# Kernel optimization log

Measured on AMD Instinct MI355X. Metric: run time of the kernel, lower is better.

The kernel has to match this reference:

```python
import jax, jax.numpy as jnp
import numpy as np

HID = 512
HEADS = 8
HEAD_DIM = HID // HEADS
B, S = 2, 4096


def setup_inputs() -> dict:
    key = jax.random.key(0)
    ks = jax.random.split(key, 11)
    sc = 0.02
    return {
        "query": jax.random.normal(ks[0], (B, S, HID), jnp.float32),
        "key": jax.random.normal(ks[1], (B, S, HID), jnp.float32),
        "value": jax.random.normal(ks[2], (B, S, HID), jnp.float32),
        "Wq": jax.random.normal(ks[3], (HID, HID), jnp.float32) * sc,
        "bq": jax.random.normal(ks[4], (HID,), jnp.float32) * sc,
        "Wk": jax.random.normal(ks[5], (HID, HID), jnp.float32) * sc,
        "bk": jax.random.normal(ks[6], (HID,), jnp.float32) * sc,
        "Wv": jax.random.normal(ks[7], (HID, HID), jnp.float32) * sc,
        "bv": jax.random.normal(ks[8], (HID,), jnp.float32) * sc,
        "Wo": jax.random.normal(ks[9], (HID, HID), jnp.float32) * sc,
        "bo": jax.random.normal(ks[10], (HID,), jnp.float32) * sc,
    }


def reference(query, key, value, Wq, bq, Wk, bk, Wv, bv, Wo, bo):
    b, s, _ = query.shape
    scale = jnp.sqrt(jnp.float32(HEAD_DIM))
    # projections (nn.Linear: x @ W.T + b)
    Q = query @ Wq.T + bq
    K = key @ Wk.T + bk
    V = value @ Wv.T + bv
    # split heads: [b, h, s, d]
    Q = Q.reshape(b, s, HEADS, HEAD_DIM).transpose(0, 2, 1, 3)
    K = K.reshape(b, s, HEADS, HEAD_DIM).transpose(0, 2, 1, 3)
    V = V.reshape(b, s, HEADS, HEAD_DIM).transpose(0, 2, 1, 3)
    # scaled dot-product attention (mask=None, dropout in eval mode = identity)
    energy = jnp.einsum('bhqd,bhkd->bhqk', Q, K) / scale
    attention = jax.nn.softmax(energy, axis=-1)
    x = jnp.einsum('bhqk,bhkd->bhqd', attention, V)
    x = x.transpose(0, 2, 1, 3).reshape(b, s, HID)
    return x @ Wo.T + bo
```

## Files before the change

### kernel.cpp

```cpp
#include <hip/hip_runtime.h>
#include <stdint.h>

#define HID 512
#define NH 8
#define HD 64
#define BATCH 2
#define SEQ 4096
#define M_TOT (BATCH*SEQ)
#define NBH (BATCH*NH)
#define SPLITK 4

typedef __attribute__((ext_vector_type(8))) short short8;
typedef __attribute__((ext_vector_type(4))) short short4v;
typedef __attribute__((ext_vector_type(4))) float floatx4;
typedef unsigned short u16;

__device__ inline u16 f2bf(float x) {
  unsigned u = __builtin_bit_cast(unsigned, x);
  unsigned r = u + 0x7fff + ((u >> 16) & 1);
  return (u16)(r >> 16);
}

__device__ inline float bf2f(u16 h) {
  unsigned u = ((unsigned)h) << 16;
  return __builtin_bit_cast(float, u);
}

__device__ inline unsigned pack_bf16(float a, float b) {
  unsigned ua = __builtin_bit_cast(unsigned, a) + 0x8000u;
  unsigned ub = __builtin_bit_cast(unsigned, b) + 0x8000u;
  return __builtin_amdgcn_perm(ub, ua, 0x07060302u);
}

__device__ inline void gll16(const void* g, void* l) {
  __builtin_amdgcn_global_load_lds((const __attribute__((address_space(1))) void*)g,
                                   (__attribute__((address_space(3))) void*)l, 16, 0, 0);
}


__global__ void cvt_all(const float* __restrict__ q, const float* __restrict__ k,
                        const float* __restrict__ v, const float* __restrict__ wq,
                        const float* __restrict__ wk, const float* __restrict__ wv,
                        const float* __restrict__ wo,
                        u16* __restrict__ xq, u16* __restrict__ xk,
                        u16* __restrict__ xv, u16* __restrict__ wb) {
  const size_t NW = (size_t)HID * HID;
  int bx = (int)blockIdx.x;
  const float* src; u16* dst; int blk;
  if (bx < 12288) {
    int seg = bx >> 12;
    blk = bx & 4095;
    src = (seg == 0) ? q : ((seg == 1) ? k : v);
    dst = (seg == 0) ? xq : ((seg == 1) ? xk : xv);
  } else {
    int w = (bx - 12288) >> 8;
    blk = (bx - 12288) & 255;
    src = (w == 0) ? wq : ((w == 1) ? wk : ((w == 2) ? wv : wo));
    dst = wb + (size_t)w * NW;
  }
  int i = (blk * 256 + (int)threadIdx.x) * 4;
  const float4 val = *(const float4*)(src + i);
  union { uint2 u; u16 h[4]; } pk;
  pk.h[0] = f2bf(val.x); pk.h[1] = f2bf(val.y);
  pk.h[2] = f2bf(val.z); pk.h[3] = f2bf(val.w);
  *(uint2*)(dst + i) = pk.u;
}

__global__ __launch_bounds__(256) void gemm_qkv(
    const u16* __restrict__ Xq, const u16* __restrict__ Xk, const u16* __restrict__ Xv,
    const u16* __restrict__ Wb,
    const float* __restrict__ bq, const float* __restrict__ bk, const float* __restrict__ bv,
    u16* __restrict__ Qp, u16* __restrict__ Kp, u16* __restrict__ Vt) {
  const int z = blockIdx.z;
  const u16* X = (z == 0) ? Xq : ((z == 1) ? Xk : Xv);
  const u16* W = Wb + (size_t)z * (HID * HID);
  const float* bias = (z == 0) ? bq : ((z == 1) ? bk : bv);

  __shared__ u16 As[128 * 32];
  __shared__ u16 Bs[128 * 32];

  const int tid = threadIdx.x;
  const int wid = tid >> 6, lane = tid & 63;
  const int wm = wid >> 1, wn = wid & 1;
  const int quad = lane >> 4, l16 = lane & 15;
  const int m0 = (int)blockIdx.x * 128, n0 = (int)blockIdx.y * 128;
  const int srow = lane >> 2;
  const int scol = (lane & 3) * 8;

  floatx4 acc[4][4];
#pragma unroll
  for (int i = 0; i < 4; i++)
#pragma unroll
    for (int j = 0; j < 4; j++) acc[i][j] = floatx4{0.f, 0.f, 0.f, 0.f};

  for (int k0 = 0; k0 < HID; k0 += 32) {
#pragma unroll
    for (int r = 0; r < 2; r++) {
      int row = r * 64 + wid * 16 + srow;
      gll16(X + (size_t)(m0 + row) * HID + k0 + scol, &As[(r * 64 + wid * 16) * 32]);
      gll16(W + (size_t)(n0 + row) * HID + k0 + scol, &Bs[(r * 64 + wid * 16) * 32]);
    }
    __syncthreads();
    short8 af[4], bf[4];
#pragma unroll
    for (int mt = 0; mt < 4; mt++)
      af[mt] = *(const short8*)&As[(wm * 64 + mt * 16 + l16) * 32 + quad * 8];
#pragma unroll
    for (int nt = 0; nt < 4; nt++)
      bf[nt] = *(const short8*)&Bs[(wn * 64 + nt * 16 + l16) * 32 + quad * 8];
#pragma unroll
    for (int mt = 0; mt < 4; mt++)
#pragma unroll
      for (int nt = 0; nt < 4; nt++)
        acc[mt][nt] = __builtin_amdgcn_mfma_f32_16x16x32_bf16(af[mt], bf[nt], acc[mt][nt], 0, 0, 0);
    __syncthreads();
  }

#pragma unroll
  for (int mt = 0; mt < 4; mt++) {
#pragma unroll
    for (int nt = 0; nt < 4; nt++) {
      int ncol = n0 + wn * 64 + nt * 16 + l16;
      float bias_v = bias[ncol];
      int h = ncol >> 6, d = ncol & 63;
#pragma unroll
      for (int r = 0; r < 4; r++) {
        int mrow = m0 + wm * 64 + mt * 16 + quad * 4 + r;
        float v = acc[mt][nt][r] + bias_v;
        int b = mrow >> 12, s = mrow & (SEQ - 1);
        size_t base = (size_t)(b * NH + h) * SEQ * HD;
        if (z == 2) {
          size_t idx = base + (size_t)(s >> 4) * 1024 + (d >> 4) * 256 + ((s >> 2) & 3) * 64 + (d & 15) * 4 + (s & 3);
          Vt[idx] = f2bf(v);
        } else {
          size_t idx = base + (size_t)(s >> 4) * 1024 + (d >> 3) * 128 + (s & 15) * 8 + (d & 7);
          if (z == 0) Qp[idx] = f2bf(v * 0.18033688f);
          else        Kp[idx] = f2bf(v);
        }
      }
    }
  }
}

__global__ __launch_bounds__(256) void gemm_out(
    const u16* __restrict__ X, const u16* __restrict__ W,
    const float* __restrict__ bias, float* __restrict__ out) {
  __shared__ u16 As[128 * 32];
  __shared__ u16 Bs[64 * 32];

  const int tid = threadIdx.x;
  const int wid = tid >> 6, lane = tid & 63;
  const int wm = wid >> 1, wn = wid & 1;
  const int quad = lane >> 4, l16 = lane & 15;
  const int m0 = (int)blockIdx.x * 128, n0 = (int)blockIdx.y * 64;
  const int srow = lane >> 2;
  const int scol = (lane & 3) * 8;

  floatx4 acc[4][2];
#pragma unroll
  for (int i = 0; i < 4; i++)
#pragma unroll
    for (int j = 0; j < 2; j++) acc[i][j] = floatx4{0.f, 0.f, 0.f, 0.f};

  for (int k0 = 0; k0 < HID; k0 += 32) {
#pragma unroll
    for (int r = 0; r < 2; r++) {
      int row = r * 64 + wid * 16 + srow;
      gll16(X + (size_t)(m0 + row) * HID + k0 + scol, &As[(r * 64 + wid * 16) * 32]);
    }
    {
      int row = wid * 16 + srow;
      gll16(W + (size_t)(n0 + row) * HID + k0 + scol, &Bs[(wid * 16) * 32]);
    }
    __syncthreads();
    short8 af[4], bf[2];
#pragma unroll
    for (int mt = 0; mt < 4; mt++)
      af[mt] = *(const short8*)&As[(wm * 64 + mt * 16 + l16) * 32 + quad * 8];
#pragma unroll
    for (int nt = 0; nt < 2; nt++)
      bf[nt] = *(const short8*)&Bs[(wn * 32 + nt * 16 + l16) * 32 + quad * 8];
#pragma unroll
    for (int mt = 0; mt < 4; mt++)
#pragma unroll
      for (int nt = 0; nt < 2; nt++)
        acc[mt][nt] = __builtin_amdgcn_mfma_f32_16x16x32_bf16(af[mt], bf[nt], acc[mt][nt], 0, 0, 0);
    __syncthreads();
  }

#pragma unroll
  for (int mt = 0; mt < 4; mt++) {
#pragma unroll
    for (int nt = 0; nt < 2; nt++) {
      int ncol = n0 + wn * 32 + nt * 16 + l16;
      float bias_v = bias[ncol];
#pragma unroll
      for (int r = 0; r < 4; r++) {
        int mrow = m0 + wm * 64 + mt * 16 + quad * 4 + r;
        out[(size_t)mrow * HID + ncol] = acc[mt][nt][r] + bias_v;
      }
    }
  }
}

__global__ __launch_bounds__(256) void attn_kernel(
    const u16* __restrict__ Qp, const u16* __restrict__ Kp,
    const u16* __restrict__ Vt, u16* __restrict__ Opb, float* __restrict__ Lp) {
  const int bh = blockIdx.y;
  const int sp = blockIdx.z;
  const int q0 = (int)blockIdx.x * 128;
  const u16* Qh = Qp + (size_t)bh * SEQ * HD;
  const u16* Kh = Kp + (size_t)bh * SEQ * HD;
  const u16* Vh = Vt + (size_t)bh * SEQ * HD;

  __shared__ u16 Ks[2][4096];
  __shared__ u16 Vs[2][4096];

  const int tid = threadIdx.x;
  const int wid = tid >> 6, lane = tid & 63;
  const int quad = lane >> 4, l16 = lane & 15;

  short8 qf[2][2];
#pragma unroll
  for (int kq = 0; kq < 2; kq++)
#pragma unroll
    for (int n = 0; n < 2; n++)
      qf[kq][n] = *(const short8*)(Qh + (size_t)(q0 / 16 + wid * 2 + n) * 1024 + (kq * 4 + quad) * 128 + l16 * 8);

  float l_part[2] = {0.f, 0.f};
  floatx4 o[2][4];
#pragma unroll
  for (int m = 0; m < 2; m++)
#pragma unroll
    for (int dt = 0; dt < 4; dt++) o[m][dt] = floatx4{0.f, 0.f, 0.f, 0.f};

  const int kv_lo = sp * (SEQ / SPLITK), kv_hi = kv_lo + SEQ / SPLITK;

  auto stage = [&](int buf, int kv0) {
    const u16* kg = Kh + (size_t)(kv0 >> 4) * 1024;
    const u16* vg = Vh + (size_t)(kv0 >> 4) * 1024;
#pragma unroll
    for (int r = 0; r < 2; r++) {
      int c = wid + r * 4;
      gll16(kg + c * 512 + lane * 8, &Ks[buf][c * 512]);
      gll16(vg + c * 512 + lane * 8, &Vs[buf][c * 512]);
    }
  };

  stage(0, kv_lo);
  __syncthreads();

  int ibuf = 0;
  for (int kv0 = kv_lo; kv0 < kv_hi; kv0 += 64) {
    if (kv0 + 64 < kv_hi) stage(ibuf ^ 1, kv0 + 64);

#pragma unroll
    for (int t = 0; t < 4; t++) {
      short8 ak0 = *(const short8*)&Ks[ibuf][t * 1024 + (0 * 4 + quad) * 128 + l16 * 8];
      short8 ak1 = *(const short8*)&Ks[ibuf][t * 1024 + (1 * 4 + quad) * 128 + l16 * 8];
      short4v vf[4];
#pragma unroll
      for (int dt = 0; dt < 4; dt++)
        vf[dt] = *(const short4v*)&Vs[ibuf][t * 1024 + dt * 256 + quad * 64 + l16 * 4];

      floatx4 st[2];
      st[0] = __builtin_amdgcn_mfma_f32_16x16x32_bf16(ak0, qf[0][0], floatx4{0.f,0.f,0.f,0.f}, 0, 0, 0);
      st[1] = __builtin_amdgcn_mfma_f32_16x16x32_bf16(ak0, qf[0][1], floatx4{0.f,0.f,0.f,0.f}, 0, 0, 0);
      st[0] = __builtin_amdgcn_mfma_f32_16x16x32_bf16(ak1, qf[1][0], st[0], 0, 0, 0);
      st[1] = __builtin_amdgcn_mfma_f32_16x16x32_bf16(ak1, qf[1][1], st[1], 0, 0, 0);

#pragma unroll
      for (int n = 0; n < 2; n++) {
        float p0 = __builtin_amdgcn_exp2f(st[n][0]);
        float p1 = __builtin_amdgcn_exp2f(st[n][1]);
        float p2 = __builtin_amdgcn_exp2f(st[n][2]);
        float p3 = __builtin_amdgcn_exp2f(st[n][3]);
        l_part[n] += (p0 + p1) + (p2 + p3);
        union { unsigned u[2]; short4v s; } pk;
        pk.u[0] = pack_bf16(p0, p1);
        pk.u[1] = pack_bf16(p2, p3);
#pragma unroll
        for (int dt = 0; dt < 4; dt++)
          o[n][dt] = __builtin_amdgcn_mfma_f32_16x16x16bf16_1k(pk.s, vf[dt], o[n][dt], 0, 0, 0);
      }
    }
    __syncthreads();
    ibuf ^= 1;
  }

#pragma unroll
  for (int n = 0; n < 2; n++) {
    l_part[n] += __shfl_xor(l_part[n], 16);
    l_part[n] += __shfl_xor(l_part[n], 32);
  }
  u16* Oph = Opb + (size_t)(sp * NBH + bh) * SEQ * HD;
  float* Lph = Lp + (size_t)(sp * NBH + bh) * SEQ;
  if (quad == 0) {
#pragma unroll
    for (int n = 0; n < 2; n++)
      Lph[q0 + wid * 32 + n * 16 + l16] = l_part[n];
  }
#pragma unroll
  for (int m = 0; m < 2; m++) {
#pragma unroll
    for (int r = 0; r < 4; r++) {
      int s = q0 + wid * 32 + m * 16 + quad * 4 + r;
#pragma unroll
      for (int dt = 0; dt < 4; dt++)
        Oph[(size_t)s * HD + dt * 16 + l16] = f2bf(o[m][dt][r]);
    }
  }
}

__global__ __launch_bounds__(256) void combine_kernel(
    const u16* __restrict__ Opb, const float* __restrict__ Lp, u16* __restrict__ Xo) {
  int idx = (int)blockIdx.x * 256 + (int)threadIdx.x;
  int e = idx * 4;
  int bh = e >> 18;
  int rem = e & 262143;
  int q = rem >> 6, d = rem & 63;
  float acc0 = 0.f, acc1 = 0.f, acc2 = 0.f, acc3 = 0.f, lsum = 0.f;
#pragma unroll
  for (int sp = 0; sp < SPLITK; sp++) {
    size_t i = ((size_t)(sp * NBH + bh) * SEQ + q) * HD + d;
    union { uint2 u; u16 h[4]; } pk;
    pk.u = *(const uint2*)(Opb + i);
    acc0 += bf2f(pk.h[0]); acc1 += bf2f(pk.h[1]);
    acc2 += bf2f(pk.h[2]); acc3 += bf2f(pk.h[3]);
    lsum += Lp[(size_t)(sp * NBH + bh) * SEQ + q];
  }
  float inv = 1.f / lsum;
  int b = bh >> 3, h = bh & 7;
  u16* dst = Xo + ((size_t)(b * SEQ + q)) * HID + h * HD + d;
  union { uint2 u; u16 hh[4]; } pk;
  pk.hh[0] = f2bf(acc0 * inv);
  pk.hh[1] = f2bf(acc1 * inv);
  pk.hh[2] = f2bf(acc2 * inv);
  pk.hh[3] = f2bf(acc3 * inv);
  *(uint2*)dst = pk.u;
}

extern "C" void kernel_launch(void* const* d_in, const int* in_sizes, int n_in,
                              void* d_out, int out_size, void* d_ws, size_t ws_size,
                              hipStream_t stream) {
  const float* q  = (const float*)d_in[0];
  const float* k  = (const float*)d_in[1];
  const float* v  = (const float*)d_in[2];
  const float* Wq = (const float*)d_in[3];
  const float* bq = (const float*)d_in[4];
  const float* Wk = (const float*)d_in[5];
  const float* bk = (const float*)d_in[6];
  const float* Wv = (const float*)d_in[7];
  const float* bv = (const float*)d_in[8];
  const float* Wo = (const float*)d_in[9];
  const float* bo = (const float*)d_in[10];

  u16* wsb = (u16*)d_ws;
  const size_t NW = (size_t)HID * HID;
  const size_t NX = (size_t)M_TOT * HID;
  u16* Wb = wsb;
  u16* Xq = wsb + 4 * NW;
  u16* Xk = Xq + NX;
  u16* Xv = Xk + NX;
  u16* Qp = Xv + NX;
  u16* Kp = Qp + NX;
  u16* Vt = Kp + NX;
  u16* Xo = Vt + NX;
  u16* Opb = Xo + NX;
  float* Lp = (float*)(Opb + (size_t)SPLITK * NBH * SEQ * HD);

  dim3 blk(256);
  cvt_all<<<dim3(13312), blk, 0, stream>>>(q, k, v, Wq, Wk, Wv, Wo, Xq, Xk, Xv, Wb);

  gemm_qkv<<<dim3(64, 4, 3), blk, 0, stream>>>(Xq, Xk, Xv, Wb, bq, bk, bv, Qp, Kp, Vt);
  attn_kernel<<<dim3(32, NBH, SPLITK), blk, 0, stream>>>(Qp, Kp, Vt, Opb, Lp);
  combine_kernel<<<dim3(4096), blk, 0, stream>>>(Opb, Lp, Xo);
  gemm_out<<<dim3(64, 8), blk, 0, stream>>>(Xo, Wb + 3 * NW, bo, (float*)d_out);
}
```

Baseline: 236.4 us.

## Fuse activation fp32-to-bf16 conversion into QKV GEMM and double attention query tile

Drops the separate conversion pass over the query, key and value activations. The QKV GEMM now loads fp32 rows directly, packs them to bf16 in registers and writes them to shared memory, which removes a full write and re-read of the bf16 copies. The attention kernel also handles 256 queries per block (64 per wave), so each staged K/V tile is reused across twice as many queries. In exchange there are more registers per wave, half as many attention blocks, and a synchronous global load in the GEMM A path instead of the async LDS load.

```diff
diff --git a/kernel.cpp b/kernel.cpp
--- a/kernel.cpp
+++ b/kernel.cpp
@@ -38,26 +38,15 @@
 }
 
 
-__global__ void cvt_all(const float* __restrict__ q, const float* __restrict__ k,
-                        const float* __restrict__ v, const float* __restrict__ wq,
-                        const float* __restrict__ wk, const float* __restrict__ wv,
-                        const float* __restrict__ wo,
-                        u16* __restrict__ xq, u16* __restrict__ xk,
-                        u16* __restrict__ xv, u16* __restrict__ wb) {
+__global__ void cvt_w(const float* __restrict__ wq, const float* __restrict__ wk,
+                      const float* __restrict__ wv, const float* __restrict__ wo,
+                      u16* __restrict__ wb) {
   const size_t NW = (size_t)HID * HID;
   int bx = (int)blockIdx.x;
-  const float* src; u16* dst; int blk;
-  if (bx < 12288) {
-    int seg = bx >> 12;
-    blk = bx & 4095;
-    src = (seg == 0) ? q : ((seg == 1) ? k : v);
-    dst = (seg == 0) ? xq : ((seg == 1) ? xk : xv);
-  } else {
-    int w = (bx - 12288) >> 8;
-    blk = (bx - 12288) & 255;
-    src = (w == 0) ? wq : ((w == 1) ? wk : ((w == 2) ? wv : wo));
-    dst = wb + (size_t)w * NW;
-  }
+  int w = bx >> 8;
+  int blk = bx & 255;
+  const float* src = (w == 0) ? wq : ((w == 1) ? wk : ((w == 2) ? wv : wo));
+  u16* dst = wb + (size_t)w * NW;
   int i = (blk * 256 + (int)threadIdx.x) * 4;
   const float4 val = *(const float4*)(src + i);
   union { uint2 u; u16 h[4]; } pk;
@@ -67,12 +56,12 @@
 }
 
 __global__ __launch_bounds__(256) void gemm_qkv(
-    const u16* __restrict__ Xq, const u16* __restrict__ Xk, const u16* __restrict__ Xv,
+    const float* __restrict__ Xq, const float* __restrict__ Xk, const float* __restrict__ Xv,
     const u16* __restrict__ Wb,
     const float* __restrict__ bq, const float* __restrict__ bk, const float* __restrict__ bv,
     u16* __restrict__ Qp, u16* __restrict__ Kp, u16* __restrict__ Vt) {
   const int z = blockIdx.z;
-  const u16* X = (z == 0) ? Xq : ((z == 1) ? Xk : Xv);
+  const float* X = (z == 0) ? Xq : ((z == 1) ? Xk : Xv);
   const u16* W = Wb + (size_t)z * (HID * HID);
   const float* bias = (z == 0) ? bq : ((z == 1) ? bk : bv);
 
@@ -86,6 +75,8 @@
   const int m0 = (int)blockIdx.x * 128, n0 = (int)blockIdx.y * 128;
   const int srow = lane >> 2;
   const int scol = (lane & 3) * 8;
+  const int arow = tid >> 1;
+  const int acol = (tid & 1) * 16;
 
   floatx4 acc[4][4];
 #pragma unroll
@@ -94,10 +85,21 @@
     for (int j = 0; j < 4; j++) acc[i][j] = floatx4{0.f, 0.f, 0.f, 0.f};
 
   for (int k0 = 0; k0 < HID; k0 += 32) {
+    const float* ap = X + (size_t)(m0 + arow) * HID + k0 + acol;
+    float4 a0 = *(const float4*)(ap + 0);
+    float4 a1 = *(const float4*)(ap + 4);
+    float4 a2 = *(const float4*)(ap + 8);
+    float4 a3 = *(const float4*)(ap + 12);
+    uint4 w0, w1;
+    w0.x = pack_bf16(a0.x, a0.y); w0.y = pack_bf16(a0.z, a0.w);
+    w0.z = pack_bf16(a1.x, a1.y); w0.w = pack_bf16(a1.z, a1.w);
+    w1.x = pack_bf16(a2.x, a2.y); w1.y = pack_bf16(a2.z, a2.w);
+    w1.z = pack_bf16(a3.x, a3.y); w1.w = pack_bf16(a3.z, a3.w);
+    *(uint4*)&As[arow * 32 + acol] = w0;
+    *(uint4*)&As[arow * 32 + acol + 8] = w1;
 #pragma unroll
     for (int r = 0; r < 2; r++) {
       int row = r * 64 + wid * 16 + srow;
-      gll16(X + (size_t)(m0 + row) * HID + k0 + scol, &As[(r * 64 + wid * 16) * 32]);
       gll16(W + (size_t)(n0 + row) * HID + k0 + scol, &Bs[(r * 64 + wid * 16) * 32]);
     }
     __syncthreads();
@@ -169,8 +171,7 @@
       gll16(X + (size_t)(m0 + row) * HID + k0 + scol, &As[(r * 64 + wid * 16) * 32]);
     }
     {
-      int row = wid * 16 + srow;
-      gll16(W + (size_t)(n0 + row) * HID + k0 + scol, &Bs[(wid * 16) * 32]);
+      gll16(W + (size_t)(n0 + wid * 16 + srow) * HID + k0 + scol, &Bs[(wid * 16) * 32]);
     }
     __syncthreads();
     short8 af[4], bf[2];
@@ -208,7 +209,7 @@
     const u16* __restrict__ Vt, u16* __restrict__ Opb, float* __restrict__ Lp) {
   const int bh = blockIdx.y;
   const int sp = blockIdx.z;
-  const int q0 = (int)blockIdx.x * 128;
+  const int q0 = (int)blockIdx.x * 256;
   const u16* Qh = Qp + (size_t)bh * SEQ * HD;
   const u16* Kh = Kp + (size_t)bh * SEQ * HD;
   const u16* Vh = Vt + (size_t)bh * SEQ * HD;
@@ -220,19 +221,19 @@
   const int wid = tid >> 6, lane = tid & 63;
   const int quad = lane >> 4, l16 = lane & 15;
 
-  short8 qf[2][2];
+  short8 qf[2][4];
 #pragma unroll
   for (int kq = 0; kq < 2; kq++)
 #pragma unroll
-    for (int n = 0; n < 2; n++)
-      qf[kq][n] = *(const short8*)(Qh + (size_t)(q0 / 16 + wid * 2 + n) * 1024 + (kq * 4 + quad) * 128 + l16 * 8);
-
-  float l_part[2] = {0.f, 0.f};
-  floatx4 o[2][4];
-#pragma unroll
-  for (int m = 0; m < 2; m++)
-#pragma unroll
-    for (int dt = 0; dt < 4; dt++) o[m][dt] = floatx4{0.f, 0.f, 0.f, 0.f};
+    for (int n = 0; n < 4; n++)
+      qf[kq][n] = *(const short8*)(Qh + (size_t)((q0 >> 4) + wid * 4 + n) * 1024 + (kq * 4 + quad) * 128 + l16 * 8);
+
+  float l_part[4] = {0.f, 0.f, 0.f, 0.f};
+  floatx4 o[4][4];
+#pragma unroll
+  for (int n = 0; n < 4; n++)
+#pragma unroll
+    for (int dt = 0; dt < 4; dt++) o[n][dt] = floatx4{0.f, 0.f, 0.f, 0.f};
 
   const int kv_lo = sp * (SEQ / SPLITK), kv_hi = kv_lo + SEQ / SPLITK;
 
@@ -263,14 +264,15 @@
       for (int dt = 0; dt < 4; dt++)
         vf[dt] = *(const short4v*)&Vs[ibuf][t * 1024 + dt * 256 + quad * 64 + l16 * 4];
 
-      floatx4 st[2];
-      st[0] = __builtin_amdgcn_mfma_f32_16x16x32_bf16(ak0, qf[0][0], floatx4{0.f,0.f,0.f,0.f}, 0, 0, 0);
-      st[1] = __builtin_amdgcn_mfma_f32_16x16x32_bf16(ak0, qf[0][1], floatx4{0.f,0.f,0.f,0.f}, 0, 0, 0);
-      st[0] = __builtin_amdgcn_mfma_f32_16x16x32_bf16(ak1, qf[1][0], st[0], 0, 0, 0);
-      st[1] = __builtin_amdgcn_mfma_f32_16x16x32_bf16(ak1, qf[1][1], st[1], 0, 0, 0);
-
-#pragma unroll
-      for (int n = 0; n < 2; n++) {
+      floatx4 st[4];
+#pragma unroll
+      for (int n = 0; n < 4; n++) {
+        st[n] = __builtin_amdgcn_mfma_f32_16x16x32_bf16(ak0, qf[0][n], floatx4{0.f,0.f,0.f,0.f}, 0, 0, 0);
+        st[n] = __builtin_amdgcn_mfma_f32_16x16x32_bf16(ak1, qf[1][n], st[n], 0, 0, 0);
+      }
+
+#pragma unroll
+      for (int n = 0; n < 4; n++) {
         float p0 = __builtin_amdgcn_exp2f(st[n][0]);
         float p1 = __builtin_amdgcn_exp2f(st[n][1]);
         float p2 = __builtin_amdgcn_exp2f(st[n][2]);
@@ -289,7 +291,7 @@
   }
 
 #pragma unroll
-  for (int n = 0; n < 2; n++) {
+  for (int n = 0; n < 4; n++) {
     l_part[n] += __shfl_xor(l_part[n], 16);
     l_part[n] += __shfl_xor(l_part[n], 32);
   }
@@ -297,17 +299,17 @@
   float* Lph = Lp + (size_t)(sp * NBH + bh) * SEQ;
   if (quad == 0) {
 #pragma unroll
-    for (int n = 0; n < 2; n++)
-      Lph[q0 + wid * 32 + n * 16 + l16] = l_part[n];
-  }
-#pragma unroll
-  for (int m = 0; m < 2; m++) {
+    for (int n = 0; n < 4; n++)
+      Lph[q0 + wid * 64 + n * 16 + l16] = l_part[n];
+  }
+#pragma unroll
+  for (int n = 0; n < 4; n++) {
 #pragma unroll
     for (int r = 0; r < 4; r++) {
-      int s = q0 + wid * 32 + m * 16 + quad * 4 + r;
+      int s = q0 + wid * 64 + n * 16 + quad * 4 + r;
 #pragma unroll
       for (int dt = 0; dt < 4; dt++)
-        Oph[(size_t)s * HD + dt * 16 + l16] = f2bf(o[m][dt][r]);
+        Oph[(size_t)s * HD + dt * 16 + l16] = f2bf(o[n][dt][r]);
     }
   }
 }
@@ -359,10 +361,7 @@
   const size_t NW = (size_t)HID * HID;
   const size_t NX = (size_t)M_TOT * HID;
   u16* Wb = wsb;
-  u16* Xq = wsb + 4 * NW;
-  u16* Xk = Xq + NX;
-  u16* Xv = Xk + NX;
-  u16* Qp = Xv + NX;
+  u16* Qp = wsb + 4 * NW;
   u16* Kp = Qp + NX;
   u16* Vt = Kp + NX;
   u16* Xo = Vt + NX;
@@ -370,10 +369,9 @@
   float* Lp = (float*)(Opb + (size_t)SPLITK * NBH * SEQ * HD);
 
   dim3 blk(256);
-  cvt_all<<<dim3(13312), blk, 0, stream>>>(q, k, v, Wq, Wk, Wv, Wo, Xq, Xk, Xv, Wb);
-
-  gemm_qkv<<<dim3(64, 4, 3), blk, 0, stream>>>(Xq, Xk, Xv, Wb, bq, bk, bv, Qp, Kp, Vt);
-  attn_kernel<<<dim3(32, NBH, SPLITK), blk, 0, stream>>>(Qp, Kp, Vt, Opb, Lp);
+  cvt_w<<<dim3(1024), blk, 0, stream>>>(Wq, Wk, Wv, Wo, Wb);
+  gemm_qkv<<<dim3(64, 4, 3), blk, 0, stream>>>(q, k, v, Wb, bq, bk, bv, Qp, Kp, Vt);
+  attn_kernel<<<dim3(16, NBH, SPLITK), blk, 0, stream>>>(Qp, Kp, Vt, Opb, Lp);
   combine_kernel<<<dim3(4096), blk, 0, stream>>>(Opb, Lp, Xo);
   gemm_out<<<dim3(64, 8), blk, 0, stream>>>(Xo, Wb + 3 * NW, bo, (float*)d_out);
 }
```

Result: no change. 237.5 us (+0.5%).
